# Performance work log

Measured on AMD Instinct MI355X. Metric: run time of the kernel, lower is better.

Reference implementation:

```python
import jax, jax.numpy as jnp
import numpy as np

N, E, G = 30000, 240000, 1000
F, H = 78, 10            # in-features, GAT heads
HID = F * H              # 780
NEG_SLOPE = 0.2


def setup_inputs() -> dict:
    key = jax.random.key(0)
    ks = jax.random.split(key, 12)
    x = jax.random.normal(ks[0], (N, F), dtype=jnp.float32)
    edge_index = jax.random.randint(ks[1], (2, E), 0, N, dtype=jnp.int32)
    batch = jnp.sort(jax.random.randint(ks[2], (N,), 0, G, dtype=jnp.int32))
    def lin(k, fan_in, shape):
        return (jax.random.normal(k, shape, dtype=jnp.float32)
                / jnp.sqrt(jnp.float32(fan_in)))
    return {
        "x": x,
        "edge_index": edge_index,
        "batch": batch,
        "W_gat": lin(ks[3], F, (F, HID)),          # GATConv lin weight
        "att_src": lin(ks[4], F, (H, F)),          # GAT attention vectors
        "att_dst": lin(ks[5], F, (H, F)),
        "b_gat": jnp.zeros((HID,), jnp.float32),
        "W_gcn": lin(ks[6], HID, (HID, HID)),
        "b_gcn": jnp.zeros((HID,), jnp.float32),
        "W1": lin(ks[7], 2 * HID, (2 * HID, 1500)),
        "b1": jnp.zeros((1500,), jnp.float32),
        "W2": lin(ks[8], 1500, (1500, 128)),
        "b2": jnp.zeros((128,), jnp.float32),
    }


def _with_self_loops(edge_index):
    loop = jnp.arange(N, dtype=edge_index.dtype)
    src = jnp.concatenate([edge_index[0], loop])
    dst = jnp.concatenate([edge_index[1], loop])
    return src, dst


def reference(x, edge_index, batch, W_gat, att_src, att_dst, b_gat,
              W_gcn, b_gcn, W1, b1, W2, b2):
    src, dst = _with_self_loops(edge_index)  # [E+N]

    # ---- GATConv(78 -> 78, heads=10, concat) ----
    h = (x @ W_gat).reshape(N, H, F)                       # [N,H,F]
    a_src = jnp.einsum('nhf,hf->nh', h, att_src)           # [N,H]
    a_dst = jnp.einsum('nhf,hf->nh', h, att_dst)
    e = jax.nn.leaky_relu(a_src[src] + a_dst[dst], NEG_SLOPE)  # [Et,H]
    # segment softmax over incoming edges of each dst node
    e_max = jax.ops.segment_max(e, dst, num_segments=N)
    e_exp = jnp.exp(e - e_max[dst])
    denom = jax.ops.segment_sum(e_exp, dst, num_segments=N)
    alpha = e_exp / denom[dst]                             # [Et,H]
    msg = h[src] * alpha[:, :, None]                       # [Et,H,F]
    out = jax.ops.segment_sum(msg, dst, num_segments=N).reshape(N, HID) + b_gat
    out = jax.nn.relu(out)

    # ---- GCNConv(780 -> 780), symmetric norm with self loops ----
    h2 = out @ W_gcn                                       # [N,HID]
    deg = jax.ops.segment_sum(jnp.ones_like(dst, jnp.float32), dst,
                              num_segments=N)
    dinv = jax.lax.rsqrt(jnp.maximum(deg, 1.0))
    norm = dinv[src] * dinv[dst]                           # [Et]
    out2 = jax.ops.segment_sum(norm[:, None] * h2[src], dst,
                               num_segments=N) + b_gcn
    out2 = jax.nn.relu(out2)

    # ---- global mean / max pool over molecules ----
    counts = jax.ops.segment_sum(jnp.ones((N,), jnp.float32), batch,
                                 num_segments=G)
    gsum = jax.ops.segment_sum(out2, batch, num_segments=G)
    gmean = gsum / jnp.maximum(counts, 1.0)[:, None]
    gmax = jax.ops.segment_max(out2, batch, num_segments=G)
    gmax = jnp.where(counts[:, None] > 0, gmax, 0.0)
    pooled = jnp.concatenate([gmean, gmax], axis=1)        # [G, 1560]

    # ---- MLP head (dropout = identity at eval) ----
    hidfc = jax.nn.relu(pooled @ W1 + b1)
    return hidfc @ W2 + b2                                 # [G, 128]
```

## Files before the change

kernel.cpp:

```cpp
#include <hip/hip_runtime.h>

#define NN 30000
#define EE 240000
#define ET 270000
#define GG 1000
#define NH 10
#define FF 78
#define HID 780
#define NEG_SLOPE 0.2f

#define LD_H 784
#define KP_GCN 800
#define NP_HID 896
#define KP_X 96
#define LD_Z 960
#define MP_N 30080
#define KP_P 1600
#define NP_W1 1536
#define LD_FC 1536
#define MP_G 1024

#define MT 128
#define NT 128
#define NBLK 30
#define EB 4
#define EBG 6

#define C_X   (MP_N * KP_X)
#define C_WE  (NH * 128 * 96)
#define C_WC  (NP_HID * KP_GCN)
#define C_W1  (NP_W1 * KP_P)
#define C_W2  (128 * LD_FC)
#define C_PB  KP_GCN
#define C_WS  (FF * 2 * NH)
#define C_IN  NN
#define C_TOT (C_X + C_WE + C_WC + C_W1 + C_W2 + C_PB + C_WS + C_IN)

typedef __bf16 bf16_8 __attribute__((ext_vector_type(8)));
typedef float f32x4 __attribute__((ext_vector_type(4)));

__device__ __forceinline__ void async_copy16(const void* g, void* l) {
  __builtin_amdgcn_global_load_lds(
      (const __attribute__((address_space(1))) void*)g,
      (__attribute__((address_space(3))) void*)l, 16, 0, 0);
}

__device__ __forceinline__ float bf2f(unsigned int bits) {
  return __uint_as_float(bits << 16);
}

template <bool OUT_BF, int KBC, bool DBUF>
__global__ __launch_bounds__(256) void mfma_gemm(
    const __bf16* __restrict__ A, const __bf16* __restrict__ BT,
    float* __restrict__ Cf, __bf16* __restrict__ Cb,
    const float* __restrict__ bias, int M, int Kp, int Nout, int ldc,
    int relu, int rp, int nct, int mtiles) {
  constexpr int NST = KBC / 32;
  constexpr int TST = KBC / 16;
  constexpr int STAGEB = (KBC / 8) * MT * 8 * 2;
  constexpr int NEED = (DBUF ? 4 : 2) * STAGEB;
  constexpr int SMEM = NEED > 32768 ? NEED : 32768;
  __shared__ char smem[SMEM];
  int rt, ct;
  if (rp > 0) {
    int bid = blockIdx.x;
    int p = bid & 7, s = bid >> 3;
    int q = s / nct;
    rt = p * rp + q;
    ct = s - q * nct;
    if (rt >= mtiles) return;
  } else {
    rt = blockIdx.y; ct = blockIdx.x;
  }
  int row0 = rt * MT, col0 = ct * NT;
  int tid = threadIdx.x;
  int lane = tid & 63, wave = tid >> 6;
  int wm = (wave & 1) * 64, wn = (wave >> 1) * 64;
  int l15 = lane & 15, quad = lane >> 4;
  f32x4 acc[4][4] = {};

  auto stage = [&](int k0, int buf) {
    char* baseA = smem + (DBUF ? buf * 2 * STAGEB : 0);
    char* baseB = baseA + STAGEB;
    for (int t = 0; t < TST; t++) {
      int base = t * 256 + wave * 64;
      int s = base + lane;
      int kc = s >> 7, r = s & 127;
      async_copy16(A + (size_t)(row0 + r) * Kp + k0 + kc * 8,
                   baseA + (size_t)base * 16);
    }
    for (int t = 0; t < TST; t++) {
      int base = t * 256 + wave * 64;
      int s = base + lane;
      int kc = s >> 7, r = s & 127;
      async_copy16(BT + (size_t)(col0 + r) * Kp + k0 + kc * 8,
                   baseB + (size_t)base * 16);
    }
  };
  auto compute = [&](int buf) {
    char* baseA = smem + (DBUF ? buf * 2 * STAGEB : 0);
    char* baseB = baseA + STAGEB;
    for (int st = 0; st < NST; st++) {
      bf16_8 af[4], bfv[4];
      for (int mt = 0; mt < 4; mt++)
        af[mt] = *(const bf16_8*)(baseA +
            (size_t)((st * 4 + quad) * MT + wm + mt * 16 + l15) * 16);
      for (int nt = 0; nt < 4; nt++)
        bfv[nt] = *(const bf16_8*)(baseB +
            (size_t)((st * 4 + quad) * MT + wn + nt * 16 + l15) * 16);
      for (int mt = 0; mt < 4; mt++)
        for (int nt = 0; nt < 4; nt++)
          acc[mt][nt] = __builtin_amdgcn_mfma_f32_16x16x32_bf16(
              af[mt], bfv[nt], acc[mt][nt], 0, 0, 0);
    }
  };

  if (DBUF) {
    int niter = Kp / KBC;
    stage(0, 0);
    for (int k = 0; k < niter; k++) {
      __syncthreads();
      if (k + 1 < niter) stage((k + 1) * KBC, (k + 1) & 1);
      compute(k & 1);
    }
    __syncthreads();
  } else {
    for (int k0 = 0; k0 < Kp; k0 += KBC) {
      stage(k0, 0);
      __syncthreads();
      compute(0);
      __syncthreads();
    }
  }

  if (OUT_BF) {
    __bf16* Cs = (__bf16*)smem;
    for (int nt = 0; nt < 4; nt++) {
      int col_l = wn + nt * 16 + l15;
      int gcol = col0 + col_l;
      bool valid = gcol < Nout;
      float bv = (valid && bias) ? bias[gcol] : 0.f;
      int ch = col_l >> 3, wi = col_l & 7;
      for (int mt = 0; mt < 4; mt++) {
        for (int r = 0; r < 4; r++) {
          int rl = wm + mt * 16 + quad * 4 + r;
          float v = 0.f;
          if (valid) {
            v = acc[mt][nt][r] + bv;
            if (relu) v = fmaxf(v, 0.f);
          }
          Cs[rl * 128 + ((ch ^ (rl & 7)) << 3) + wi] = (__bf16)v;
        }
      }
    }
    __syncthreads();
    for (int idx = tid; idx < MT * 16; idx += 256) {
      int rl = idx >> 4, ch = idx & 15;
      int grow = row0 + rl, gcol = col0 + ch * 8;
      if (grow < M && gcol + 8 <= ldc)
        *(bf16_8*)(Cb + (size_t)grow * ldc + gcol) =
            *(const bf16_8*)&Cs[rl * 128 + ((ch ^ (rl & 7)) << 3)];
    }
  } else {
    for (int nt = 0; nt < 4; nt++) {
      int col = col0 + wn + nt * 16 + l15;
      if (col >= ldc) continue;
      bool valid = col < Nout;
      float bv = (valid && bias) ? bias[col] : 0.f;
      for (int mt = 0; mt < 4; mt++) {
        int rbase = row0 + wm + mt * 16 + quad * 4;
        for (int r = 0; r < 4; r++) {
          int row = rbase + r;
          if (row >= M) continue;
          float v = 0.f;
          if (valid) {
            v = acc[mt][nt][r] + bv;
            if (relu) v = fmaxf(v, 0.f);
          }
          Cf[(size_t)row * ldc + col] = v;
        }
      }
    }
  }
}

__global__ __launch_bounds__(256) void gemm_head(
    const __bf16* __restrict__ z, const __bf16* __restrict__ WE,
    const float* __restrict__ pb, __bf16* __restrict__ C) {
  __shared__ char smem[49152];
  __bf16* As = (__bf16*)smem;
  __bf16* Bs = (__bf16*)(smem + 24576);
  int head = blockIdx.x;
  int row0 = blockIdx.y * MT;
  int col0 = 80 * head;
  int tid = threadIdx.x;
  int lane = tid & 63, wave = tid >> 6;
  int wm = (wave & 1) * 64, wn = (wave >> 1) * 64;
  int l15 = lane & 15, quad = lane >> 4;

  for (int t = 0; t < 6; t++) {
    int base = t * 256 + wave * 64;
    int s = base + lane;
    int kc = s >> 7, r = s & 127;
    async_copy16(z + (size_t)(row0 + r) * LD_Z + 96 * head + kc * 8,
                 (char*)As + (size_t)base * 16);
  }
  for (int t = 0; t < 6; t++) {
    int base = t * 256 + wave * 64;
    int s = base + lane;
    int kc = s >> 7, r = s & 127;
    async_copy16(WE + (size_t)head * 128 * 96 + (size_t)r * 96 + kc * 8,
                 (char*)Bs + (size_t)base * 16);
  }
  __syncthreads();

  f32x4 acc[4][4] = {};
  for (int st = 0; st < 3; st++) {
    bf16_8 af[4], bfv[4];
    for (int mt = 0; mt < 4; mt++)
      af[mt] = *(const bf16_8*)&As[(size_t)((st * 4 + quad) * 128 + wm + mt * 16 + l15) * 8];
    for (int nt = 0; nt < 4; nt++)
      bfv[nt] = *(const bf16_8*)&Bs[(size_t)((st * 4 + quad) * 128 + wn + nt * 16 + l15) * 8];
    for (int mt = 0; mt < 4; mt++)
      for (int nt = 0; nt < 4; nt++)
        acc[mt][nt] = __builtin_amdgcn_mfma_f32_16x16x32_bf16(
            af[mt], bfv[nt], acc[mt][nt], 0, 0, 0);
  }
  __syncthreads();

  __bf16* Cs = (__bf16*)smem;
  for (int nt = 0; nt < 4; nt++) {
    int col_l = wn + nt * 16 + l15;
    bool valid = col_l < 78;
    float bv = valid ? pb[col0 + col_l] : 0.f;
    int ch = col_l >> 3, wi = col_l & 7;
    for (int mt = 0; mt < 4; mt++) {
      for (int r = 0; r < 4; r++) {
        int rl = wm + mt * 16 + quad * 4 + r;
        float v = valid ? fmaxf(acc[mt][nt][r] + bv, 0.f) : 0.f;
        Cs[rl * 128 + ((ch ^ (rl & 7)) << 3) + wi] = (__bf16)v;
      }
    }
  }
  __syncthreads();
  for (int idx = tid; idx < MT * 10; idx += 256) {
    int rl = idx / 10, ch = idx - rl * 10;
    int grow = row0 + rl;
    if (grow < NN)
      *(bf16_8*)(C + (size_t)grow * KP_GCN + col0 + ch * 8) =
          *(const bf16_8*)&Cs[rl * 128 + ((ch ^ (rl & 7)) << 3)];
  }
}

__global__ __launch_bounds__(256) void prep_kernel(
    const float* __restrict__ x, const float* __restrict__ W_gat,
    const float* __restrict__ att_src, const float* __restrict__ att_dst,
    const float* __restrict__ W_gcn, const float* __restrict__ W1,
    const float* __restrict__ W2, const float* __restrict__ b_gat,
    __bf16* __restrict__ x_bf, __bf16* __restrict__ WE,
    __bf16* __restrict__ WgcnT, __bf16* __restrict__ W1T,
    __bf16* __restrict__ W2T, float* __restrict__ pb,
    float* __restrict__ wsd, int* __restrict__ cnt, int* __restrict__ fill,
    int* __restrict__ lo, int* __restrict__ hi) {
  int gid = blockIdx.x * 256 + threadIdx.x;
  if (gid < C_X) {
    int n = gid / KP_X, k = gid - n * KP_X;
    x_bf[gid] = (__bf16)((n < NN && k < FF) ? x[(size_t)n * FF + k] : 0.f);
    return;
  }
  gid -= C_X;
  if (gid < C_WE) {
    int h = gid / (128 * 96);
    int rem = gid - h * 128 * 96;
    int n = rem / 96, k = rem - n * 96;
    WE[gid] = (__bf16)((n < FF && k < FF)
                           ? W_gat[(size_t)k * HID + h * FF + n] : 0.f);
    return;
  }
  gid -= C_WE;
  if (gid < C_WC) {
    int n = gid / KP_GCN, kp = gid - n * KP_GCN;
    int hh = kp / 80, f = kp - hh * 80;
    WgcnT[gid] = (__bf16)((n < HID && f < FF)
                              ? W_gcn[(size_t)(FF * hh + f) * HID + n] : 0.f);
    return;
  }
  gid -= C_WC;
  if (gid < C_W1) {
    int n = gid / KP_P, k = gid - n * KP_P;
    W1T[gid] = (__bf16)((n < 1500 && k < 2 * HID) ? W1[(size_t)k * 1500 + n] : 0.f);
    return;
  }
  gid -= C_W1;
  if (gid < C_W2) {
    int n = gid / LD_FC, k = gid - n * LD_FC;
    W2T[gid] = (__bf16)((n < 128 && k < 1500) ? W2[(size_t)k * 128 + n] : 0.f);
    return;
  }
  gid -= C_W2;
  if (gid < C_PB) {
    int hh = gid / 80, f = gid - hh * 80;
    pb[gid] = (f < FF) ? b_gat[FF * hh + f] : 0.f;
    return;
  }
  gid -= C_PB;
  if (gid < C_WS) {
    int k = gid / (2 * NH), c = gid - k * (2 * NH);
    int h = (c < NH) ? c : c - NH;
    const float* att = (c < NH) ? att_src : att_dst;
    float s = 0.f;
    for (int f = 0; f < FF; f++)
      s += W_gat[(size_t)k * HID + h * FF + f] * att[h * FF + f];
    wsd[k * 2 * NH + c] = s;
    return;
  }
  gid -= C_WS;
  if (gid < C_IN) {
    cnt[gid] = 0; fill[gid] = 0;
    if (gid < GG) { lo[gid] = NN; hi[gid] = 0; }
  }
}

__device__ __forceinline__ void edge_sd(const int* __restrict__ ei, int t,
                                        int& s, int& d) {
  if (t < EE) { s = ei[t]; d = ei[EE + t]; }
  else        { s = t - EE; d = t - EE; }
}

__global__ __launch_bounds__(256) void adot_count_kernel(
    const float* __restrict__ x, const float* __restrict__ wsd,
    float* __restrict__ a_src, float* __restrict__ a_dst,
    const int* __restrict__ ei, const int* __restrict__ batch,
    int* __restrict__ cnt, int* __restrict__ lo, int* __restrict__ hi) {
  __shared__ float w_s[FF * 2 * NH];
  for (int i = threadIdx.x; i < FF * 2 * NH; i += 256) w_s[i] = wsd[i];
  int gid = blockIdx.x * 256 + threadIdx.x;
  if (gid < ET) { int s, d; edge_sd(ei, gid, s, d); atomicAdd(&cnt[d], 1); }
  if (gid < NN) {
    int g = batch[gid];
    atomicMin(&lo[g], gid);
    atomicMax(&hi[g], gid + 1);
  }
  __syncthreads();
  if (gid >= NN * 2 * NH) return;
  int n = gid / (2 * NH), c = gid - n * (2 * NH);
  float s = 0.f;
  for (int k = 0; k < FF; k++) s += x[(size_t)n * FF + k] * w_s[k * 2 * NH + c];
  if (c < NH) a_src[n * NH + c] = s;
  else        a_dst[n * NH + (c - NH)] = s;
}

__global__ __launch_bounds__(1024) void scan1_kernel(
    const int* __restrict__ cnt, int* __restrict__ row_ptr,
    int* __restrict__ partial) {
  __shared__ int buf[1024];
  int i = blockIdx.x * 1024 + threadIdx.x;
  int v = (i < NN) ? cnt[i] : 0;
  buf[threadIdx.x] = v;
  __syncthreads();
  for (int off = 1; off < 1024; off <<= 1) {
    int t = (threadIdx.x >= off) ? buf[threadIdx.x - off] : 0;
    __syncthreads();
    buf[threadIdx.x] += t;
    __syncthreads();
  }
  if (i < NN) row_ptr[i] = buf[threadIdx.x] - v;
  if (threadIdx.x == 1023) partial[blockIdx.x] = buf[1023];
}

__global__ __launch_bounds__(256) void scan3_kernel(
    int* __restrict__ row_ptr, const int* __restrict__ partial,
    const int* __restrict__ cnt, float* __restrict__ dinv) {
  __shared__ int pre[NBLK];
  if (threadIdx.x == 0) {
    int run = 0;
    for (int b = 0; b < NBLK; b++) { pre[b] = run; run += partial[b]; }
  }
  __syncthreads();
  int i = blockIdx.x * 256 + threadIdx.x;
  if (i < NN) {
    row_ptr[i] += pre[i >> 10];
    dinv[i] = rsqrtf((float)max(cnt[i], 1));
  }
  if (i == 0) row_ptr[NN] = ET;
}

__global__ void scatter_kernel(const int* __restrict__ ei,
                               const int* __restrict__ row_ptr,
                               int* __restrict__ fill,
                               int* __restrict__ col_src,
                               int* __restrict__ dst_csr) {
  int t = blockIdx.x * blockDim.x + threadIdx.x;
  if (t >= ET) return;
  int s, d; edge_sd(ei, t, s, d);
  int pos = row_ptr[d] + atomicAdd(&fill[d], 1);
  col_src[pos] = s;
  dst_csr[pos] = d;
}

__global__ void pexp_kernel(const int* __restrict__ col_src,
                            const int* __restrict__ dst_csr,
                            const float* __restrict__ a_src,
                            const float* __restrict__ a_dst,
                            float* __restrict__ p_csr) {
  int t = blockIdx.x * blockDim.x + threadIdx.x;
  if (t >= ET) return;
  int s = col_src[t], d = dst_csr[t];
#pragma unroll
  for (int h = 0; h < NH; h++) {
    float v = a_src[s * NH + h] + a_dst[d * NH + h];
    v = (v > 0.f) ? v : v * NEG_SLOPE;
    p_csr[(size_t)t * NH + h] = __expf(v);
  }
}

__global__ __launch_bounds__(256) void gat_x_aggr_kernel(
    const int* __restrict__ row_ptr, const int* __restrict__ col_src,
    const float* __restrict__ p_csr, const __bf16* __restrict__ x_bf,
    __bf16* __restrict__ z) {
  int wave = threadIdx.x >> 6;
  int lane = threadIdx.x & 63;
  int d = blockIdx.x * 2 + (wave >> 1);
  int idx = (wave & 1) * 64 + lane;
  int beg = row_ptr[d], end = row_ptr[d + 1];

  if (idx < 100) {
    int h = idx / 10, j = idx - h * 10;
    int k0 = 8 * j;
    float acc[8] = {};
    float sum = 0.f;
    for (int e = beg; e < end; e += EB) {
      int sidx[EB]; float pp[EB];
#pragma unroll
      for (int q = 0; q < EB; q++) {
        bool ok = (e + q < end);
        int ee = ok ? e + q : beg;
        sidx[q] = col_src[ee];
        float p = p_csr[(size_t)ee * NH + h];
        pp[q] = ok ? p : 0.f;
      }
      uint4 rr[EB];
#pragma unroll
      for (int q = 0; q < EB; q++)
        rr[q] = *(const uint4*)(x_bf + (size_t)sidx[q] * KP_X + k0);
#pragma unroll
      for (int q = 0; q < EB; q++) {
        sum += pp[q];
        unsigned int w[4] = {rr[q].x, rr[q].y, rr[q].z, rr[q].w};
#pragma unroll
        for (int k = 0; k < 8; k++) {
          unsigned int bits = (k & 1) ? (w[k >> 1] >> 16) : (w[k >> 1] & 0xffffu);
          acc[k] += bf2f(bits) * pp[q];
        }
      }
    }
    float inv = 1.f / sum;
    bf16_8 o;
#pragma unroll
    for (int k = 0; k < 8; k++) {
      float val = (k0 + k < FF) ? acc[k] * inv : 0.f;
      o[k] = (__bf16)val;
    }
    *(bf16_8*)(z + (size_t)d * LD_Z + 96 * h + k0) = o;
  } else if (idx < 120) {
    int t = idx - 100;
    int h = t >> 1;
    int k0 = 80 + 8 * (t & 1);
    bf16_8 zz = {};
    *(bf16_8*)(z + (size_t)d * LD_Z + 96 * h + k0) = zz;
  }
}

__global__ __launch_bounds__(256) void gcn_aggr_kernel(
    const int* __restrict__ row_ptr, const int* __restrict__ col_src,
    const float* __restrict__ dinv, const __bf16* __restrict__ h2,
    const float* __restrict__ b_gcn, __bf16* __restrict__ out2) {
  int wave = threadIdx.x >> 6;
  int lane = threadIdx.x & 63;
  int d = blockIdx.x * 2 + (wave >> 1);
  int half = wave & 1;
  int beg = row_ptr[d], end = row_ptr[d + 1];
  if (lane >= 49) return;
  int f0 = half * 392 + 8 * lane;
  float dv = dinv[d];
  float acc[8] = {};
  for (int e = beg; e < end; e += EBG) {
    int sidx[EBG]; float ww[EBG];
#pragma unroll
    for (int j = 0; j < EBG; j++) {
      bool ok = (e + j < end);
      int ee = ok ? e + j : beg;
      int s = col_src[ee];
      sidx[j] = s;
      ww[j] = ok ? dinv[s] * dv : 0.f;
    }
    uint4 rr[EBG];
#pragma unroll
    for (int j = 0; j < EBG; j++)
      rr[j] = *(const uint4*)(h2 + (size_t)sidx[j] * LD_H + f0);
#pragma unroll
    for (int j = 0; j < EBG; j++) {
      unsigned int wb[4] = {rr[j].x, rr[j].y, rr[j].z, rr[j].w};
#pragma unroll
      for (int k = 0; k < 8; k++) {
        unsigned int bits = (k & 1) ? (wb[k >> 1] >> 16) : (wb[k >> 1] & 0xffffu);
        acc[k] += bf2f(bits) * ww[j];
      }
    }
  }
  bf16_8 o0;
#pragma unroll
  for (int k = 0; k < 8; k++) {
    int f = f0 + k;
    float val = (f < HID) ? fmaxf(acc[k] + b_gcn[f], 0.f) : 0.f;
    o0[k] = (__bf16)val;
  }
  *(bf16_8*)(out2 + (size_t)d * LD_H + f0) = o0;
}

__global__ __launch_bounds__(128) void pool_kernel(
    const __bf16* __restrict__ out2, const int* __restrict__ lo,
    const int* __restrict__ hi, __bf16* __restrict__ pooled) {
  int g = blockIdx.x;
  int l = lo[g], h = hi[g];
  int t = threadIdx.x;
  if (t >= 98) {
    if (t < 103) {
      int base = 1560 + (t - 98) * 8;
      for (int k = 0; k < 8; k++) pooled[(size_t)g * KP_P + base + k] = (__bf16)0.f;
    }
    return;
  }
  int f0 = 8 * t;
  float s[8] = {}, mx[8];
#pragma unroll
  for (int k = 0; k < 8; k++) mx[k] = -1e30f;
  for (int n = l; n < h; n++) {
    uint4 r = *(const uint4*)(out2 + (size_t)n * LD_H + f0);
    unsigned int w[4] = {r.x, r.y, r.z, r.w};
#pragma unroll
    for (int k = 0; k < 8; k++) {
      unsigned int bits = (k & 1) ? (w[k >> 1] >> 16) : (w[k >> 1] & 0xffffu);
      float v = bf2f(bits);
      s[k] += v;
      mx[k] = fmaxf(mx[k], v);
    }
  }
  float invc = (h > l) ? 1.f / (float)(h - l) : 0.f;
#pragma unroll
  for (int k = 0; k < 8; k++) {
    int f = f0 + k;
    if (f >= HID) continue;
    float mean = (h > l) ? s[k] * invc : 0.f;
    float mxx  = (h > l) ? mx[k] : 0.f;
    pooled[(size_t)g * KP_P + f] = (__bf16)mean;
    pooled[(size_t)g * KP_P + HID + f] = (__bf16)mxx;
  }
}

extern "C" void kernel_launch(void* const* d_in, const int* in_sizes, int n_in,
                              void* d_out, int out_size, void* d_ws,
                              size_t ws_size, hipStream_t stream) {
  const float* x        = (const float*)d_in[0];
  const int*   edge_idx = (const int*)d_in[1];
  const int*   batch    = (const int*)d_in[2];
  const float* W_gat    = (const float*)d_in[3];
  const float* att_src  = (const float*)d_in[4];
  const float* att_dst  = (const float*)d_in[5];
  const float* b_gat    = (const float*)d_in[6];
  const float* W_gcn    = (const float*)d_in[7];
  const float* b_gcn    = (const float*)d_in[8];
  const float* W1       = (const float*)d_in[9];
  const float* b1       = (const float*)d_in[10];
  const float* W2       = (const float*)d_in[11];
  const float* b2       = (const float*)d_in[12];
  float* out = (float*)d_out;
  (void)in_sizes; (void)n_in; (void)out_size; (void)ws_size;

  char* ws = (char*)d_ws;
  size_t off = 0;
  auto alloc = [&](size_t bytes) -> void* {
    void* p = ws + off;
    off += (bytes + 255) & ~(size_t)255;
    return p;
  };
  char*  bufR     = (char*)alloc((size_t)MP_N * KP_GCN * 2);
  __bf16* A_bf    = (__bf16*)bufR;
  __bf16* out2b   = (__bf16*)bufR;
  __bf16* z_bf    = (__bf16*)alloc((size_t)MP_N * LD_Z * 2);
  __bf16* h2_bf   = (__bf16*)alloc((size_t)MP_N * LD_H * 2);
  __bf16* x_bf    = (__bf16*)alloc((size_t)MP_N * KP_X * 2);
  __bf16* WE      = (__bf16*)alloc((size_t)NH * 128 * 96 * 2);
  __bf16* WgcnT   = (__bf16*)alloc((size_t)NP_HID * KP_GCN * 2);
  __bf16* W1T     = (__bf16*)alloc((size_t)NP_W1 * KP_P * 2);
  __bf16* W2T     = (__bf16*)alloc((size_t)128 * LD_FC * 2);
  __bf16* pooled  = (__bf16*)alloc((size_t)MP_G * KP_P * 2);
  __bf16* hidfc   = (__bf16*)alloc((size_t)MP_G * LD_FC * 2);
  float* pb       = (float*)alloc((size_t)KP_GCN * 4);
  float* wsd      = (float*)alloc((size_t)FF * 2 * NH * 4);
  float* a_src_b  = (float*)alloc((size_t)NN * NH * 4);
  float* a_dst_b  = (float*)alloc((size_t)NN * NH * 4);
  float* p_csr    = (float*)alloc((size_t)ET * NH * 4);
  int*   cnt      = (int*)alloc((size_t)NN * 4);
  int*   fill     = (int*)alloc((size_t)NN * 4);
  int*   row_ptr  = (int*)alloc((size_t)(NN + 1) * 4);
  int*   col_src  = (int*)alloc((size_t)ET * 4);
  int*   dst_csr  = (int*)alloc((size_t)ET * 4);
  int*   partial  = (int*)alloc((size_t)NBLK * 4);
  int*   lo       = (int*)alloc((size_t)GG * 4);
  int*   hi       = (int*)alloc((size_t)GG * 4);
  float* dinv     = (float*)alloc((size_t)NN * 4);

  prep_kernel<<<(C_TOT + 255) / 256, 256, 0, stream>>>(
      x, W_gat, att_src, att_dst, W_gcn, W1, W2, b_gat, x_bf, WE, WgcnT, W1T,
      W2T, pb, wsd, cnt, fill, lo, hi);

  adot_count_kernel<<<(NN * 2 * NH + 255) / 256, 256, 0, stream>>>(
      x, wsd, a_src_b, a_dst_b, edge_idx, batch, cnt, lo, hi);

  scan1_kernel<<<NBLK, 1024, 0, stream>>>(cnt, row_ptr, partial);
  scan3_kernel<<<(NN + 255) / 256, 256, 0, stream>>>(row_ptr, partial, cnt,
                                                     dinv);
  scatter_kernel<<<(ET + 255) / 256, 256, 0, stream>>>(edge_idx, row_ptr,
                                                       fill, col_src, dst_csr);
  pexp_kernel<<<(ET + 255) / 256, 256, 0, stream>>>(col_src, dst_csr,
                                                    a_src_b, a_dst_b, p_csr);

  gat_x_aggr_kernel<<<NN / 2, 256, 0, stream>>>(row_ptr, col_src, p_csr, x_bf,
                                                z_bf);
  gemm_head<<<dim3(NH, MP_N / MT), 256, 0, stream>>>(z_bf, WE, pb, A_bf);
  {
    mfma_gemm<true, 32, true><<<dim3(8 * 30 * 7), 256, 0, stream>>>(
        A_bf, WgcnT, nullptr, h2_bf, nullptr, NN, KP_GCN, HID, LD_H, 0,
        30, 7, MP_N / MT);
  }
  gcn_aggr_kernel<<<NN / 2, 256, 0, stream>>>(row_ptr, col_src, dinv, h2_bf,
                                              b_gcn, out2b);

  pool_kernel<<<GG, 128, 0, stream>>>(out2b, lo, hi, pooled);

  {
    dim3 grid(NP_W1 / NT, MP_G / MT);
    mfma_gemm<true, 64, true><<<grid, 256, 0, stream>>>(
        pooled, W1T, nullptr, hidfc, b1, GG, KP_P, 1500, LD_FC, 1, 0, 0, 0);
  }
  {
    dim3 grid(1, MP_G / MT);
    mfma_gemm<false, 64, true><<<grid, 256, 0, stream>>>(
        hidfc, W2T, out, nullptr, b2, GG, LD_FC, 128, 128, 0, 0, 0, 0);
  }
}
```

Before: 523.7 us.

## Fuse edge attention exp into GAT aggregation and drop p_csr buffer

Removes the separate pexp kernel and its per-edge p_csr buffer (ET x 10 floats), recomputing leaky-relu and exp of the attention logits inline in the GAT aggregation from a_src/a_dst. This also drops the dst_csr array written by scatter. Separately, the GAT edge batch grows from 4 to 6 and the GCN aggregation uses packed float2 accumulation. The cost is redundant exp work, since each head's value is recomputed by the 10 lanes that share it.

```diff
diff --git a/kernel.cpp b/kernel.cpp
--- a/kernel.cpp
+++ b/kernel.cpp
@@ -23,7 +23,7 @@
 #define MT 128
 #define NT 128
 #define NBLK 30
-#define EB 4
+#define EB 6
 #define EBG 6
 
 #define C_X   (MP_N * KP_X)
@@ -38,6 +38,7 @@
 
 typedef __bf16 bf16_8 __attribute__((ext_vector_type(8)));
 typedef float f32x4 __attribute__((ext_vector_type(4)));
+typedef float f32x2 __attribute__((ext_vector_type(2)));
 
 __device__ __forceinline__ void async_copy16(const void* g, void* l) {
   __builtin_amdgcn_global_load_lds(
@@ -388,36 +389,18 @@
 __global__ void scatter_kernel(const int* __restrict__ ei,
                                const int* __restrict__ row_ptr,
                                int* __restrict__ fill,
-                               int* __restrict__ col_src,
-                               int* __restrict__ dst_csr) {
+                               int* __restrict__ col_src) {
   int t = blockIdx.x * blockDim.x + threadIdx.x;
   if (t >= ET) return;
   int s, d; edge_sd(ei, t, s, d);
   int pos = row_ptr[d] + atomicAdd(&fill[d], 1);
   col_src[pos] = s;
-  dst_csr[pos] = d;
-}
-
-__global__ void pexp_kernel(const int* __restrict__ col_src,
-                            const int* __restrict__ dst_csr,
-                            const float* __restrict__ a_src,
-                            const float* __restrict__ a_dst,
-                            float* __restrict__ p_csr) {
-  int t = blockIdx.x * blockDim.x + threadIdx.x;
-  if (t >= ET) return;
-  int s = col_src[t], d = dst_csr[t];
-#pragma unroll
-  for (int h = 0; h < NH; h++) {
-    float v = a_src[s * NH + h] + a_dst[d * NH + h];
-    v = (v > 0.f) ? v : v * NEG_SLOPE;
-    p_csr[(size_t)t * NH + h] = __expf(v);
-  }
 }
 
 __global__ __launch_bounds__(256) void gat_x_aggr_kernel(
     const int* __restrict__ row_ptr, const int* __restrict__ col_src,
-    const float* __restrict__ p_csr, const __bf16* __restrict__ x_bf,
-    __bf16* __restrict__ z) {
+    const float* __restrict__ a_src, const float* __restrict__ a_dst,
+    const __bf16* __restrict__ x_bf, __bf16* __restrict__ z) {
   int wave = threadIdx.x >> 6;
   int lane = threadIdx.x & 63;
   int d = blockIdx.x * 2 + (wave >> 1);
@@ -427,6 +410,7 @@
   if (idx < 100) {
     int h = idx / 10, j = idx - h * 10;
     int k0 = 8 * j;
+    float ad = a_dst[d * NH + h];
     float acc[8] = {};
     float sum = 0.f;
     for (int e = beg; e < end; e += EB) {
@@ -435,9 +419,11 @@
       for (int q = 0; q < EB; q++) {
         bool ok = (e + q < end);
         int ee = ok ? e + q : beg;
-        sidx[q] = col_src[ee];
-        float p = p_csr[(size_t)ee * NH + h];
-        pp[q] = ok ? p : 0.f;
+        int s = col_src[ee];
+        sidx[q] = s;
+        float v = a_src[s * NH + h] + ad;
+        v = (v > 0.f) ? v : v * NEG_SLOPE;
+        pp[q] = ok ? __expf(v) : 0.f;
       }
       uint4 rr[EB];
 #pragma unroll
@@ -483,7 +469,7 @@
   if (lane >= 49) return;
   int f0 = half * 392 + 8 * lane;
   float dv = dinv[d];
-  float acc[8] = {};
+  f32x2 acc2[4] = {};
   for (int e = beg; e < end; e += EBG) {
     int sidx[EBG]; float ww[EBG];
 #pragma unroll
@@ -500,11 +486,12 @@
       rr[j] = *(const uint4*)(h2 + (size_t)sidx[j] * LD_H + f0);
 #pragma unroll
     for (int j = 0; j < EBG; j++) {
-      unsigned int wb[4] = {rr[j].x, rr[j].y, rr[j].z, rr[j].w};
-#pragma unroll
-      for (int k = 0; k < 8; k++) {
-        unsigned int bits = (k & 1) ? (wb[k >> 1] >> 16) : (wb[k >> 1] & 0xffffu);
-        acc[k] += bf2f(bits) * ww[j];
+      bf16_8 bv = *(const bf16_8*)&rr[j];
+      f32x2 w2 = {ww[j], ww[j]};
+#pragma unroll
+      for (int p = 0; p < 4; p++) {
+        f32x2 f = {(float)bv[2 * p], (float)bv[2 * p + 1]};
+        acc2[p] += f * w2;
       }
     }
   }
@@ -512,7 +499,8 @@
 #pragma unroll
   for (int k = 0; k < 8; k++) {
     int f = f0 + k;
-    float val = (f < HID) ? fmaxf(acc[k] + b_gcn[f], 0.f) : 0.f;
+    float a = acc2[k >> 1][k & 1];
+    float val = (f < HID) ? fmaxf(a + b_gcn[f], 0.f) : 0.f;
     o0[k] = (__bf16)val;
   }
   *(bf16_8*)(out2 + (size_t)d * LD_H + f0) = o0;
@@ -600,12 +588,10 @@
   float* wsd      = (float*)alloc((size_t)FF * 2 * NH * 4);
   float* a_src_b  = (float*)alloc((size_t)NN * NH * 4);
   float* a_dst_b  = (float*)alloc((size_t)NN * NH * 4);
-  float* p_csr    = (float*)alloc((size_t)ET * NH * 4);
   int*   cnt      = (int*)alloc((size_t)NN * 4);
   int*   fill     = (int*)alloc((size_t)NN * 4);
   int*   row_ptr  = (int*)alloc((size_t)(NN + 1) * 4);
   int*   col_src  = (int*)alloc((size_t)ET * 4);
-  int*   dst_csr  = (int*)alloc((size_t)ET * 4);
   int*   partial  = (int*)alloc((size_t)NBLK * 4);
   int*   lo       = (int*)alloc((size_t)GG * 4);
   int*   hi       = (int*)alloc((size_t)GG * 4);
@@ -622,12 +608,10 @@
   scan3_kernel<<<(NN + 255) / 256, 256, 0, stream>>>(row_ptr, partial, cnt,
                                                      dinv);
   scatter_kernel<<<(ET + 255) / 256, 256, 0, stream>>>(edge_idx, row_ptr,
-                                                       fill, col_src, dst_csr);
-  pexp_kernel<<<(ET + 255) / 256, 256, 0, stream>>>(col_src, dst_csr,
-                                                    a_src_b, a_dst_b, p_csr);
-
-  gat_x_aggr_kernel<<<NN / 2, 256, 0, stream>>>(row_ptr, col_src, p_csr, x_bf,
-                                                z_bf);
+                                                       fill, col_src);
+
+  gat_x_aggr_kernel<<<NN / 2, 256, 0, stream>>>(row_ptr, col_src, a_src_b,
+                                                a_dst_b, x_bf, z_bf);
   gemm_head<<<dim3(NH, MP_N / MT), 256, 0, stream>>>(z_bf, WE, pb, A_bf);
   {
     mfma_gemm<true, 32, true><<<dim3(8 * 30 * 7), 256, 0, stream>>>(
```

Result: slower. 547.6 us (+4.5%).
